# Kernel tuning notes

Hardware: AMD Instinct MI355X
Metric: run time of the kernel (lower is better)

Reference implementation:

```python
import jax, jax.numpy as jnp
import numpy as np
import math

B, T, P, E, H = 4, 64, 256, 512, 8
D = E // H
LN_EPS = 1e-5


def setup_inputs() -> dict:
    key = jax.random.key(0)
    ks = jax.random.split(key, 6)
    s = 0.02  # weight init scale
    return {
        "x": jax.random.normal(ks[0], (B, T, P, E), jnp.float32),
        "Wq": jax.random.normal(ks[1], (E, E), jnp.float32) * s,
        "bq": jnp.zeros((E,), jnp.float32),
        "Wk": jax.random.normal(ks[2], (E, E), jnp.float32) * s,
        "bk": jnp.zeros((E,), jnp.float32),
        "Wv": jax.random.normal(ks[3], (E, E), jnp.float32) * s,
        "bv": jnp.zeros((E,), jnp.float32),
        "Wo": jax.random.normal(ks[4], (E, E), jnp.float32) * s,
        "bo": jnp.zeros((E,), jnp.float32),
        "ln_g": jnp.ones((E,), jnp.float32),
        "ln_b": jnp.zeros((E,), jnp.float32),
    }


def _proj(x, W, b):
    # torch nn.Linear: y = x @ W.T + b
    return jnp.einsum('btpe,fe->btpf', x, W) + b


def _heads(y):
    # b t p (h d) -> b p h t d
    b, t, p, e = y.shape
    return y.reshape(b, t, p, H, D).transpose(0, 2, 3, 1, 4)


def reference(x, Wq, bq, Wk, bk, Wv, bv, Wo, bo, ln_g, ln_b):
    b, t, p, e = x.shape
    q = _heads(_proj(x, Wq, bq))  # [B,P,H,T,D]
    k = _heads(_proj(x, Wk, bk))
    v = _heads(_proj(x, Wv, bv))

    scores = jnp.einsum('bphtd,bphsd->bphts', q, k) / math.sqrt(D)
    causal_mask = jnp.triu(jnp.ones((t, t), dtype=bool), k=1)  # True above diag
    scores = jnp.where(causal_mask, -jnp.inf, scores)
    attn = jax.nn.softmax(scores, axis=-1)
    o = jnp.einsum('bphts,bphsd->bphtd', attn, v)

    # b p h t d -> b t p (h d)
    o = o.transpose(0, 3, 1, 2, 4).reshape(b, t, p, e)
    attn_out = jnp.einsum('btpe,fe->btpf', o, Wo) + bo

    y = x + attn_out
    # AdaptiveNormalizer with conditioning=None -> plain LayerNorm over E
    mu = jnp.mean(y, axis=-1, keepdims=True)
    var = jnp.var(y, axis=-1, keepdims=True)
    return (y - mu) * jax.lax.rsqrt(var + LN_EPS) * ln_g + ln_b
```

## Files before the change

### kernel.cpp

```cpp
#include <hip/hip_runtime.h>
#include <stdint.h>

#define B_ 4
#define T_ 64
#define P_ 256
#define E_ 512
#define H_ 8
#define D_ 64
#define NF 1536
#define MCH 16384

typedef unsigned short u16;
typedef __attribute__((ext_vector_type(8))) __bf16 bf16x8;
typedef __attribute__((ext_vector_type(4))) float f32x4;

__device__ __forceinline__ u16 f2bf(float x) {
  union { float f; uint32_t u; } a; a.f = x;
  uint32_t u = a.u;
  uint32_t r = (u + 0x7FFFu + ((u >> 16) & 1u)) >> 16;
  return (u16)r;
}

__device__ __forceinline__ bf16x8 ld8(const u16* p) {
  union { uint4 u; bf16x8 b; } t;
  t.u = *reinterpret_cast<const uint4*>(p);
  return t.b;
}

typedef __attribute__((address_space(3))) void lds_void;
typedef __attribute__((address_space(1))) void g_void;
__device__ __forceinline__ void gl_lds16(const void* g, void* l) {
  __builtin_amdgcn_global_load_lds((g_void*)g, (lds_void*)l, 16, 0, 0);
}

__device__ __forceinline__ f32x4 mfma16(bf16x8 a, bf16x8 b, f32x4 c) {
  return __builtin_amdgcn_mfma_f32_16x16x32_bf16(a, b, c, 0, 0, 0);
}

__global__ void cvt_bf16(const float* __restrict__ src, u16* __restrict__ dst, int n8) {
  int i = blockIdx.x * blockDim.x + threadIdx.x;
  if (i >= n8) return;
  const float4* s = reinterpret_cast<const float4*>(src) + (size_t)i * 2;
  float4 a = s[0], b = s[1];
  union { u16 u[8]; uint4 v; } t;
  t.u[0] = f2bf(a.x); t.u[1] = f2bf(a.y); t.u[2] = f2bf(a.z); t.u[3] = f2bf(a.w);
  t.u[4] = f2bf(b.x); t.u[5] = f2bf(b.y); t.u[6] = f2bf(b.z); t.u[7] = f2bf(b.w);
  reinterpret_cast<uint4*>(dst)[i] = t.v;
}

__global__ __launch_bounds__(256) void k1_qkv(
    const u16* __restrict__ xbf,
    const u16* __restrict__ wqkv,
    const float* __restrict__ bq, const float* __restrict__ bk, const float* __restrict__ bv,
    u16* __restrict__ qkv)
{
  __shared__ u16 As[128 * 64];
  __shared__ u16 Bs[128 * 64];
  const int tid = threadIdx.x;
  const int lane = tid & 63;
  const int wid = tid >> 6;
  const int m0 = blockIdx.y * 128;
  const int n0 = blockIdx.x * 128;
  const int wm = (wid >> 1) * 64;
  const int wn = (wid & 1) * 64;
  const int g4 = lane >> 4;

  f32x4 acc[4][4];
#pragma unroll
  for (int i = 0; i < 4; i++)
#pragma unroll
    for (int j = 0; j < 4; j++) { f32x4 z = {0.f, 0.f, 0.f, 0.f}; acc[i][j] = z; }

  const u16* ga = xbf + (size_t)m0 * E_;
  const u16* gb = wqkv + (size_t)n0 * E_;
  const int lrow = lane >> 3;
  const int lcol = (lane & 7) * 8;

  for (int kt = 0; kt < E_ / 64; ++kt) {
    const int k0 = kt * 64;
    __syncthreads();
#pragma unroll
    for (int p = 0; p < 4; ++p) {
      const int ch = wid * 4 + p;
      const int r = ch * 8 + lrow;
      gl_lds16(ga + (size_t)r * E_ + k0 + lcol, As + ch * 512);
      gl_lds16(gb + (size_t)r * E_ + k0 + lcol, Bs + ch * 512);
    }
    __syncthreads();
#pragma unroll
    for (int ks = 0; ks < 2; ++ks) {
      const int fc = ks * 32 + g4 * 8;
      bf16x8 af[4], bfr[4];
#pragma unroll
      for (int mi = 0; mi < 4; mi++) af[mi] = ld8(As + (wm + mi * 16 + (lane & 15)) * 64 + fc);
#pragma unroll
      for (int ni = 0; ni < 4; ni++) bfr[ni] = ld8(Bs + (wn + ni * 16 + (lane & 15)) * 64 + fc);
#pragma unroll
      for (int mi = 0; mi < 4; mi++)
#pragma unroll
        for (int ni = 0; ni < 4; ni++)
          acc[mi][ni] = mfma16(af[mi], bfr[ni], acc[mi][ni]);
    }
  }
#pragma unroll
  for (int ni = 0; ni < 4; ni++) {
    const int fcol = n0 + wn + ni * 16 + (lane & 15);
    const float bias = fcol < 512 ? bq[fcol] : (fcol < 1024 ? bk[fcol - 512] : bv[fcol - 1024]);
#pragma unroll
    for (int mi = 0; mi < 4; mi++)
#pragma unroll
      for (int r = 0; r < 4; r++) {
        const int row = m0 + wm + mi * 16 + g4 * 4 + r;
        qkv[(size_t)row * NF + fcol] = f2bf(acc[mi][ni][r] + bias);
      }
  }
}

__global__ __launch_bounds__(256) void k2_attn(
    const u16* __restrict__ qkv,
    u16* __restrict__ o)
{
  __shared__ u16 Pl[4][64 * 72];
  const int tid = threadIdx.x, lane = tid & 63, wid = tid >> 6;
  const int gw = blockIdx.x * 4 + wid;
  const int h = gw & 7, p = gw >> 3;
  const int g4 = lane >> 4;
  const size_t ts = (size_t)P_ * NF;
  const u16* qb = qkv + (size_t)p * NF + h * D_;
  const u16* kb = qb + 512;
  const u16* vb = qb + 1024;

  bf16x8 qf[4][2], kf[4][2];
#pragma unroll
  for (int i = 0; i < 4; i++)
#pragma unroll
    for (int ks = 0; ks < 2; ks++) {
      const int rr = i * 16 + (lane & 15);
      const int dc = ks * 32 + g4 * 8;
      qf[i][ks] = ld8(qb + (size_t)rr * ts + dc);
      kf[i][ks] = ld8(kb + (size_t)rr * ts + dc);
    }
  f32x4 S[4][4];
#pragma unroll
  for (int i = 0; i < 4; i++)
#pragma unroll
    for (int j = 0; j < 4; j++) { f32x4 z = {0.f, 0.f, 0.f, 0.f}; S[i][j] = z; }
#pragma unroll
  for (int ks = 0; ks < 2; ks++)
#pragma unroll
    for (int mi = 0; mi < 4; mi++)
#pragma unroll
      for (int ni = 0; ni < 4; ni++)
        S[mi][ni] = mfma16(qf[mi][ks], kf[ni][ks], S[mi][ni]);

  u16* pw = &Pl[wid][0];
#pragma unroll
  for (int mi = 0; mi < 4; mi++)
#pragma unroll
    for (int r = 0; r < 4; r++) {
      const int t = mi * 16 + g4 * 4 + r;
      float v[4]; float mx = -1e30f;
#pragma unroll
      for (int ni = 0; ni < 4; ni++) {
        const int s = ni * 16 + (lane & 15);
        v[ni] = (s <= t) ? S[mi][ni][r] * 0.125f : -1e30f;
        mx = fmaxf(mx, v[ni]);
      }
      mx = fmaxf(mx, __shfl_xor(mx, 1));
      mx = fmaxf(mx, __shfl_xor(mx, 2));
      mx = fmaxf(mx, __shfl_xor(mx, 4));
      mx = fmaxf(mx, __shfl_xor(mx, 8));
      float sum = 0.f; float pv[4];
#pragma unroll
      for (int ni = 0; ni < 4; ni++) {
        const int s = ni * 16 + (lane & 15);
        pv[ni] = (s <= t) ? __expf(v[ni] - mx) : 0.f;
        sum += pv[ni];
      }
      sum += __shfl_xor(sum, 1);
      sum += __shfl_xor(sum, 2);
      sum += __shfl_xor(sum, 4);
      sum += __shfl_xor(sum, 8);
      const float inv = 1.0f / sum;
#pragma unroll
      for (int ni = 0; ni < 4; ni++) {
        const int s = ni * 16 + (lane & 15);
        pw[t * 72 + s] = f2bf(pv[ni] * inv);
      }
    }
  __syncthreads();

  f32x4 O[4][4];
#pragma unroll
  for (int i = 0; i < 4; i++)
#pragma unroll
    for (int j = 0; j < 4; j++) { f32x4 z = {0.f, 0.f, 0.f, 0.f}; O[i][j] = z; }
#pragma unroll
  for (int ks = 0; ks < 2; ks++) {
    bf16x8 pa[4], vf[4];
#pragma unroll
    for (int mi = 0; mi < 4; mi++)
      pa[mi] = ld8(pw + (mi * 16 + (lane & 15)) * 72 + ks * 32 + g4 * 8);
#pragma unroll
    for (int ni = 0; ni < 4; ni++) {
      union { u16 u[8]; bf16x8 b; } tv;
#pragma unroll
      for (int j = 0; j < 8; j++) {
        const int s = ks * 32 + g4 * 8 + j;
        tv.u[j] = vb[(size_t)s * ts + ni * 16 + (lane & 15)];
      }
      vf[ni] = tv.b;
    }
#pragma unroll
    for (int mi = 0; mi < 4; mi++)
#pragma unroll
      for (int ni = 0; ni < 4; ni++)
        O[mi][ni] = mfma16(pa[mi], vf[ni], O[mi][ni]);
  }
#pragma unroll
  for (int mi = 0; mi < 4; mi++)
#pragma unroll
    for (int ni = 0; ni < 4; ni++)
#pragma unroll
      for (int r = 0; r < 4; r++) {
        const int t = mi * 16 + g4 * 4 + r;
        const int d = ni * 16 + (lane & 15);
        o[((size_t)t * P_ + p) * E_ + h * D_ + d] = f2bf(O[mi][ni][r]);
      }
}

__global__ __launch_bounds__(256) void k3_out(
    const u16* __restrict__ obf,
    const u16* __restrict__ wo,
    const float* __restrict__ bo,
    const float* __restrict__ x,
    const float* __restrict__ lng, const float* __restrict__ lnb,
    float* __restrict__ out)
{
  __shared__ u16 As[32 * 32];
  __shared__ u16 Bs[512 * 32];
  __shared__ float redS[32][4];
  __shared__ float redQ[32][4];
  const int tid = threadIdx.x, lane = tid & 63, wid = tid >> 6;
  const int m0 = blockIdx.x * 32;
  const int g4 = lane >> 4;
  const int lr = lane >> 2;
  const int lc = (lane & 3) * 8;

  f32x4 acc[2][8];
#pragma unroll
  for (int i = 0; i < 2; i++)
#pragma unroll
    for (int j = 0; j < 8; j++) { f32x4 z = {0.f, 0.f, 0.f, 0.f}; acc[i][j] = z; }

  const u16* ga = obf + (size_t)m0 * E_;

  for (int kt = 0; kt < 16; ++kt) {
    const int k0 = kt * 32;
    __syncthreads();
    if (wid < 2) {
      gl_lds16(ga + (size_t)(wid * 16 + lr) * E_ + k0 + lc, As + wid * 512);
    }
#pragma unroll
    for (int pass = 0; pass < 8; ++pass) {
      const int ch = wid * 8 + pass;
      gl_lds16(wo + (size_t)(ch * 16 + lr) * E_ + k0 + lc, Bs + ch * 512);
    }
    __syncthreads();
    const int fc = g4 * 8;
    bf16x8 af[2], bfr[8];
#pragma unroll
    for (int mi = 0; mi < 2; mi++) af[mi] = ld8(As + (mi * 16 + (lane & 15)) * 32 + fc);
#pragma unroll
    for (int ni = 0; ni < 8; ni++) bfr[ni] = ld8(Bs + (wid * 128 + ni * 16 + (lane & 15)) * 32 + fc);
#pragma unroll
    for (int mi = 0; mi < 2; mi++)
#pragma unroll
      for (int ni = 0; ni < 8; ni++)
        acc[mi][ni] = mfma16(af[mi], bfr[ni], acc[mi][ni]);
  }

  float gg[8], bb[8], bof[8];
#pragma unroll
  for (int ni = 0; ni < 8; ni++) {
    const int f = wid * 128 + ni * 16 + (lane & 15);
    gg[ni] = lng[f]; bb[ni] = lnb[f]; bof[ni] = bo[f];
  }
#pragma unroll
  for (int mi = 0; mi < 2; mi++)
#pragma unroll
    for (int r = 0; r < 4; r++) {
      const int n = m0 + mi * 16 + g4 * 4 + r;
#pragma unroll
      for (int ni = 0; ni < 8; ni++) {
        const int f = wid * 128 + ni * 16 + (lane & 15);
        acc[mi][ni][r] += bof[ni] + x[(size_t)n * E_ + f];
      }
    }
#pragma unroll
  for (int mi = 0; mi < 2; mi++)
#pragma unroll
    for (int r = 0; r < 4; r++) {
      float s = 0.f, q = 0.f;
#pragma unroll
      for (int ni = 0; ni < 8; ni++) { const float y = acc[mi][ni][r]; s += y; q += y * y; }
      s += __shfl_xor(s, 1); q += __shfl_xor(q, 1);
      s += __shfl_xor(s, 2); q += __shfl_xor(q, 2);
      s += __shfl_xor(s, 4); q += __shfl_xor(q, 4);
      s += __shfl_xor(s, 8); q += __shfl_xor(q, 8);
      if ((lane & 15) == 0) {
        const int rl = mi * 16 + g4 * 4 + r;
        redS[rl][wid] = s; redQ[rl][wid] = q;
      }
    }
  __syncthreads();
#pragma unroll
  for (int mi = 0; mi < 2; mi++)
#pragma unroll
    for (int r = 0; r < 4; r++) {
      const int rl = mi * 16 + g4 * 4 + r;
      const float Sx = redS[rl][0] + redS[rl][1] + redS[rl][2] + redS[rl][3];
      const float Qx = redQ[rl][0] + redQ[rl][1] + redQ[rl][2] + redQ[rl][3];
      const float mean = Sx * (1.0f / 512.0f);
      const float var = Qx * (1.0f / 512.0f) - mean * mean;
      const float rs = rsqrtf(var + 1e-5f);
      const int n = m0 + rl;
#pragma unroll
      for (int ni = 0; ni < 8; ni++) {
        const int f = wid * 128 + ni * 16 + (lane & 15);
        out[(size_t)n * E_ + f] = (acc[mi][ni][r] - mean) * rs * gg[ni] + bb[ni];
      }
    }
}

extern "C" void kernel_launch(void* const* d_in, const int* in_sizes, int n_in,
                              void* d_out, int out_size, void* d_ws, size_t ws_size,
                              hipStream_t stream) {
  const float* x   = (const float*)d_in[0];
  const float* Wq  = (const float*)d_in[1];
  const float* bq  = (const float*)d_in[2];
  const float* Wk  = (const float*)d_in[3];
  const float* bk  = (const float*)d_in[4];
  const float* Wv  = (const float*)d_in[5];
  const float* bv  = (const float*)d_in[6];
  const float* Wo  = (const float*)d_in[7];
  const float* bo  = (const float*)d_in[8];
  const float* lng = (const float*)d_in[9];
  const float* lnb = (const float*)d_in[10];
  float* out = (float*)d_out;

  uint8_t* ws = (uint8_t*)d_ws;
  u16* xbf  = (u16*)(ws);
  u16* qkvc = (u16*)(ws + 16777216);
  u16* obf  = (u16*)(ws + 67108864);
  u16* wqkv = (u16*)(ws + 83886080);
  u16* wobf = (u16*)(ws + 85458944);

  cvt_bf16<<<128, 256, 0, stream>>>(Wq, wqkv,               E_ * E_ / 8);
  cvt_bf16<<<128, 256, 0, stream>>>(Wk, wqkv + E_ * E_,     E_ * E_ / 8);
  cvt_bf16<<<128, 256, 0, stream>>>(Wv, wqkv + 2 * E_ * E_, E_ * E_ / 8);
  cvt_bf16<<<128, 256, 0, stream>>>(Wo, wobf,               E_ * E_ / 8);

  for (int b = 0; b < B_; ++b) {
    const float* xb = x + (size_t)b * MCH * E_;
    cvt_bf16<<<4096, 256, 0, stream>>>(xb, xbf, MCH * E_ / 8);
    k1_qkv<<<dim3(12, 128), 256, 0, stream>>>(xbf, wqkv, bq, bk, bv, qkvc);
    k2_attn<<<512, 256, 0, stream>>>(qkvc, obf);
    k3_out<<<512, 256, 0, stream>>>(obf, wobf, bo, xb, lng, lnb, out + (size_t)b * MCH * E_);
  }
}
```

Baseline: 426.9 us.

## Double-buffer GEMM tiles, enlarge out-proj tile, batch all launches when workspace allows

Measured after the change: 433.4 us. No clear change (+1.5%).

```diff
diff --git a/kernel.cpp b/kernel.cpp
--- a/kernel.cpp
+++ b/kernel.cpp
@@ -48,14 +48,30 @@
   reinterpret_cast<uint4*>(dst)[i] = t.v;
 }
 
+__global__ void cvt_w(const float* __restrict__ Wq, const float* __restrict__ Wk,
+                      const float* __restrict__ Wv, const float* __restrict__ Wo,
+                      u16* __restrict__ wqkv, u16* __restrict__ wobf) {
+  int idx = blockIdx.x * blockDim.x + threadIdx.x;
+  int w = idx >> 15;
+  int off = idx & 32767;
+  const float* s = (w == 0) ? Wq : (w == 1) ? Wk : (w == 2) ? Wv : Wo;
+  const float4* sp = reinterpret_cast<const float4*>(s) + (size_t)off * 2;
+  float4 a = sp[0], b = sp[1];
+  union { u16 u[8]; uint4 v; } t;
+  t.u[0] = f2bf(a.x); t.u[1] = f2bf(a.y); t.u[2] = f2bf(a.z); t.u[3] = f2bf(a.w);
+  t.u[4] = f2bf(b.x); t.u[5] = f2bf(b.y); t.u[6] = f2bf(b.z); t.u[7] = f2bf(b.w);
+  if (w < 3) reinterpret_cast<uint4*>(wqkv)[w * 32768 + off] = t.v;
+  else       reinterpret_cast<uint4*>(wobf)[off] = t.v;
+}
+
 __global__ __launch_bounds__(256) void k1_qkv(
     const u16* __restrict__ xbf,
     const u16* __restrict__ wqkv,
     const float* __restrict__ bq, const float* __restrict__ bk, const float* __restrict__ bv,
     u16* __restrict__ qkv)
 {
-  __shared__ u16 As[128 * 64];
-  __shared__ u16 Bs[128 * 64];
+  __shared__ u16 As[2][128 * 64];
+  __shared__ u16 Bs[2][128 * 64];
   const int tid = threadIdx.x;
   const int lane = tid & 63;
   const int wid = tid >> 6;
@@ -63,7 +79,9 @@
   const int n0 = blockIdx.x * 128;
   const int wm = (wid >> 1) * 64;
   const int wn = (wid & 1) * 64;
-  const int g4 = lane >> 4;
+  const int g4 = lane >> 4, l15 = lane & 15;
+  const int lrow = lane >> 3;
+  const int lcol = (lane & 7) * 8;
 
   f32x4 acc[4][4];
 #pragma unroll
@@ -73,38 +91,43 @@
 
   const u16* ga = xbf + (size_t)m0 * E_;
   const u16* gb = wqkv + (size_t)n0 * E_;
-  const int lrow = lane >> 3;
-  const int lcol = (lane & 7) * 8;
-
-  for (int kt = 0; kt < E_ / 64; ++kt) {
+
+  auto stage = [&](int buf, int kt) {
     const int k0 = kt * 64;
-    __syncthreads();
 #pragma unroll
     for (int p = 0; p < 4; ++p) {
       const int ch = wid * 4 + p;
       const int r = ch * 8 + lrow;
-      gl_lds16(ga + (size_t)r * E_ + k0 + lcol, As + ch * 512);
-      gl_lds16(gb + (size_t)r * E_ + k0 + lcol, Bs + ch * 512);
-    }
-    __syncthreads();
+      gl_lds16(ga + (size_t)r * E_ + k0 + lcol, &As[buf][ch * 512]);
+      gl_lds16(gb + (size_t)r * E_ + k0 + lcol, &Bs[buf][ch * 512]);
+    }
+  };
+
+  stage(0, 0);
+  __syncthreads();
+  int cur = 0;
+  for (int kt = 0; kt < 8; ++kt) {
+    if (kt < 7) stage(cur ^ 1, kt + 1);
 #pragma unroll
     for (int ks = 0; ks < 2; ++ks) {
       const int fc = ks * 32 + g4 * 8;
       bf16x8 af[4], bfr[4];
 #pragma unroll
-      for (int mi = 0; mi < 4; mi++) af[mi] = ld8(As + (wm + mi * 16 + (lane & 15)) * 64 + fc);
-#pragma unroll
-      for (int ni = 0; ni < 4; ni++) bfr[ni] = ld8(Bs + (wn + ni * 16 + (lane & 15)) * 64 + fc);
+      for (int mi = 0; mi < 4; mi++) af[mi] = ld8(&As[cur][(wm + mi * 16 + l15) * 64 + fc]);
+#pragma unroll
+      for (int ni = 0; ni < 4; ni++) bfr[ni] = ld8(&Bs[cur][(wn + ni * 16 + l15) * 64 + fc]);
 #pragma unroll
       for (int mi = 0; mi < 4; mi++)
 #pragma unroll
         for (int ni = 0; ni < 4; ni++)
           acc[mi][ni] = mfma16(af[mi], bfr[ni], acc[mi][ni]);
     }
+    __syncthreads();
+    cur ^= 1;
   }
 #pragma unroll
   for (int ni = 0; ni < 4; ni++) {
-    const int fcol = n0 + wn + ni * 16 + (lane & 15);
+    const int fcol = n0 + wn + ni * 16 + l15;
     const float bias = fcol < 512 ? bq[fcol] : (fcol < 1024 ? bk[fcol - 512] : bv[fcol - 1024]);
 #pragma unroll
     for (int mi = 0; mi < 4; mi++)
@@ -123,12 +146,15 @@
   __shared__ u16 Pl[4][64 * 72];
   const int tid = threadIdx.x, lane = tid & 63, wid = tid >> 6;
   const int gw = blockIdx.x * 4 + wid;
-  const int h = gw & 7, p = gw >> 3;
+  const int b = gw >> 11;
+  const int g = gw & 2047;
+  const int h = g & 7, p = g >> 3;
   const int g4 = lane >> 4;
   const size_t ts = (size_t)P_ * NF;
-  const u16* qb = qkv + (size_t)p * NF + h * D_;
+  const u16* qb = qkv + (size_t)b * MCH * NF + (size_t)p * NF + h * D_;
   const u16* kb = qb + 512;
   const u16* vb = qb + 1024;
+  u16* ob = o + (size_t)b * MCH * E_;
 
   bf16x8 qf[4][2], kf[4][2];
 #pragma unroll
@@ -225,11 +251,11 @@
       for (int r = 0; r < 4; r++) {
         const int t = mi * 16 + g4 * 4 + r;
         const int d = ni * 16 + (lane & 15);
-        o[((size_t)t * P_ + p) * E_ + h * D_ + d] = f2bf(O[mi][ni][r]);
-      }
-}
-
-__global__ __launch_bounds__(256) void k3_out(
+        ob[((size_t)t * P_ + p) * E_ + h * D_ + d] = f2bf(O[mi][ni][r]);
+      }
+}
+
+__global__ __launch_bounds__(512) void k3_out(
     const u16* __restrict__ obf,
     const u16* __restrict__ wo,
     const float* __restrict__ bo,
@@ -237,97 +263,103 @@
     const float* __restrict__ lng, const float* __restrict__ lnb,
     float* __restrict__ out)
 {
-  __shared__ u16 As[32 * 32];
-  __shared__ u16 Bs[512 * 32];
-  __shared__ float redS[32][4];
-  __shared__ float redQ[32][4];
+  __shared__ u16 As[2][128 * 32];
+  __shared__ u16 Bs[2][512 * 32];
+  __shared__ float redS[128][8];
+  __shared__ float redQ[128][8];
   const int tid = threadIdx.x, lane = tid & 63, wid = tid >> 6;
-  const int m0 = blockIdx.x * 32;
-  const int g4 = lane >> 4;
+  const int m0 = blockIdx.x * 128;
+  const int g4 = lane >> 4, l15 = lane & 15;
   const int lr = lane >> 2;
   const int lc = (lane & 3) * 8;
 
-  f32x4 acc[2][8];
-#pragma unroll
-  for (int i = 0; i < 2; i++)
-#pragma unroll
-    for (int j = 0; j < 8; j++) { f32x4 z = {0.f, 0.f, 0.f, 0.f}; acc[i][j] = z; }
+  f32x4 acc[8][4];
+#pragma unroll
+  for (int i = 0; i < 8; i++)
+#pragma unroll
+    for (int j = 0; j < 4; j++) { f32x4 z = {0.f, 0.f, 0.f, 0.f}; acc[i][j] = z; }
 
   const u16* ga = obf + (size_t)m0 * E_;
 
+  auto stage = [&](int buf, int kt) {
+    const int k0 = kt * 32;
+    gl_lds16(ga + (size_t)(wid * 16 + lr) * E_ + k0 + lc, &As[buf][wid * 512]);
+#pragma unroll
+    for (int p = 0; p < 4; ++p) {
+      const int ch = wid * 4 + p;
+      gl_lds16(wo + (size_t)(ch * 16 + lr) * E_ + k0 + lc, &Bs[buf][ch * 512]);
+    }
+  };
+
+  stage(0, 0);
+  __syncthreads();
+  int cur = 0;
   for (int kt = 0; kt < 16; ++kt) {
-    const int k0 = kt * 32;
+    if (kt < 15) stage(cur ^ 1, kt + 1);
+    const int fc = g4 * 8;
+    bf16x8 af[8], bfr[4];
+#pragma unroll
+    for (int mi = 0; mi < 8; mi++) af[mi] = ld8(&As[cur][(mi * 16 + l15) * 32 + fc]);
+#pragma unroll
+    for (int ni = 0; ni < 4; ni++) bfr[ni] = ld8(&Bs[cur][(wid * 64 + ni * 16 + l15) * 32 + fc]);
+#pragma unroll
+    for (int mi = 0; mi < 8; mi++)
+#pragma unroll
+      for (int ni = 0; ni < 4; ni++)
+        acc[mi][ni] = mfma16(af[mi], bfr[ni], acc[mi][ni]);
     __syncthreads();
-    if (wid < 2) {
-      gl_lds16(ga + (size_t)(wid * 16 + lr) * E_ + k0 + lc, As + wid * 512);
-    }
-#pragma unroll
-    for (int pass = 0; pass < 8; ++pass) {
-      const int ch = wid * 8 + pass;
-      gl_lds16(wo + (size_t)(ch * 16 + lr) * E_ + k0 + lc, Bs + ch * 512);
-    }
-    __syncthreads();
-    const int fc = g4 * 8;
-    bf16x8 af[2], bfr[8];
-#pragma unroll
-    for (int mi = 0; mi < 2; mi++) af[mi] = ld8(As + (mi * 16 + (lane & 15)) * 32 + fc);
-#pragma unroll
-    for (int ni = 0; ni < 8; ni++) bfr[ni] = ld8(Bs + (wid * 128 + ni * 16 + (lane & 15)) * 32 + fc);
-#pragma unroll
-    for (int mi = 0; mi < 2; mi++)
-#pragma unroll
-      for (int ni = 0; ni < 8; ni++)
-        acc[mi][ni] = mfma16(af[mi], bfr[ni], acc[mi][ni]);
-  }
-
-  float gg[8], bb[8], bof[8];
-#pragma unroll
-  for (int ni = 0; ni < 8; ni++) {
-    const int f = wid * 128 + ni * 16 + (lane & 15);
+    cur ^= 1;
+  }
+
+  float gg[4], bb[4], bof[4];
+#pragma unroll
+  for (int ni = 0; ni < 4; ni++) {
+    const int f = wid * 64 + ni * 16 + l15;
     gg[ni] = lng[f]; bb[ni] = lnb[f]; bof[ni] = bo[f];
   }
 #pragma unroll
-  for (int mi = 0; mi < 2; mi++)
+  for (int mi = 0; mi < 8; mi++)
 #pragma unroll
     for (int r = 0; r < 4; r++) {
       const int n = m0 + mi * 16 + g4 * 4 + r;
 #pragma unroll
-      for (int ni = 0; ni < 8; ni++) {
-        const int f = wid * 128 + ni * 16 + (lane & 15);
+      for (int ni = 0; ni < 4; ni++) {
+        const int f = wid * 64 + ni * 16 + l15;
         acc[mi][ni][r] += bof[ni] + x[(size_t)n * E_ + f];
       }
     }
 #pragma unroll
-  for (int mi = 0; mi < 2; mi++)
+  for (int mi = 0; mi < 8; mi++)
 #pragma unroll
     for (int r = 0; r < 4; r++) {
       float s = 0.f, q = 0.f;
 #pragma unroll
-      for (int ni = 0; ni < 8; ni++) { const float y = acc[mi][ni][r]; s += y; q += y * y; }
+      for (int ni = 0; ni < 4; ni++) { const float y = acc[mi][ni][r]; s += y; q += y * y; }
       s += __shfl_xor(s, 1); q += __shfl_xor(q, 1);
       s += __shfl_xor(s, 2); q += __shfl_xor(q, 2);
       s += __shfl_xor(s, 4); q += __shfl_xor(q, 4);
       s += __shfl_xor(s, 8); q += __shfl_xor(q, 8);
-      if ((lane & 15) == 0) {
+      if (l15 == 0) {
         const int rl = mi * 16 + g4 * 4 + r;
         redS[rl][wid] = s; redQ[rl][wid] = q;
       }
     }
   __syncthreads();
 #pragma unroll
-  for (int mi = 0; mi < 2; mi++)
+  for (int mi = 0; mi < 8; mi++)
 #pragma unroll
     for (int r = 0; r < 4; r++) {
       const int rl = mi * 16 + g4 * 4 + r;
-      const float Sx = redS[rl][0] + redS[rl][1] + redS[rl][2] + redS[rl][3];
-      const float Qx = redQ[rl][0] + redQ[rl][1] + redQ[rl][2] + redQ[rl][3];
+      float Sx = 0.f, Qx = 0.f;
+#pragma unroll
+      for (int w = 0; w < 8; w++) { Sx += redS[rl][w]; Qx += redQ[rl][w]; }
       const float mean = Sx * (1.0f / 512.0f);
       const float var = Qx * (1.0f / 512.0f) - mean * mean;
       const float rs = rsqrtf(var + 1e-5f);
       const int n = m0 + rl;
 #pragma unroll
-      for (int ni = 0; ni < 8; ni++) {
-        const int f = wid * 128 + ni * 16 + (lane & 15);
+      for (int ni = 0; ni < 4; ni++) {
+        const int f = wid * 64 + ni * 16 + l15;
         out[(size_t)n * E_ + f] = (acc[mi][ni][r] - mean) * rs * gg[ni] + bb[ni];
       }
     }
@@ -348,24 +380,35 @@
   const float* lng = (const float*)d_in[9];
   const float* lnb = (const float*)d_in[10];
   float* out = (float*)d_out;
-
   uint8_t* ws = (uint8_t*)d_ws;
-  u16* xbf  = (u16*)(ws);
-  u16* qkvc = (u16*)(ws + 16777216);
-  u16* obf  = (u16*)(ws + 67108864);
-  u16* wqkv = (u16*)(ws + 83886080);
-  u16* wobf = (u16*)(ws + 85458944);
-
-  cvt_bf16<<<128, 256, 0, stream>>>(Wq, wqkv,               E_ * E_ / 8);
-  cvt_bf16<<<128, 256, 0, stream>>>(Wk, wqkv + E_ * E_,     E_ * E_ / 8);
-  cvt_bf16<<<128, 256, 0, stream>>>(Wv, wqkv + 2 * E_ * E_, E_ * E_ / 8);
-  cvt_bf16<<<128, 256, 0, stream>>>(Wo, wobf,               E_ * E_ / 8);
-
-  for (int b = 0; b < B_; ++b) {
-    const float* xb = x + (size_t)b * MCH * E_;
-    cvt_bf16<<<4096, 256, 0, stream>>>(xb, xbf, MCH * E_ / 8);
-    k1_qkv<<<dim3(12, 128), 256, 0, stream>>>(xbf, wqkv, bq, bk, bv, qkvc);
-    k2_attn<<<512, 256, 0, stream>>>(qkvc, obf);
-    k3_out<<<512, 256, 0, stream>>>(obf, wobf, bo, xb, lng, lnb, out + (size_t)b * MCH * E_);
-  }
-}
+
+  const size_t NEED_BIG = 270532608ULL;
+  if (ws_size >= NEED_BIG) {
+    u16* wqkv = (u16*)(ws);
+    u16* wobf = (u16*)(ws + 1572864);
+    u16* xbf  = (u16*)(ws + 2097152);
+    u16* qkvc = (u16*)(ws + 69206016);
+    u16* obf  = xbf;
+
+    cvt_w<<<512, 256, 0, stream>>>(Wq, Wk, Wv, Wo, wqkv, wobf);
+    cvt_bf16<<<16384, 256, 0, stream>>>(x, xbf, B_ * MCH * E_ / 8);
+    k1_qkv<<<dim3(12, 512), 256, 0, stream>>>(xbf, wqkv, bq, bk, bv, qkvc);
+    k2_attn<<<2048, 256, 0, stream>>>(qkvc, obf);
+    k3_out<<<512, 512, 0, stream>>>(obf, wobf, bo, x, lng, lnb, out);
+  } else {
+    u16* xbf  = (u16*)(ws);
+    u16* qkvc = (u16*)(ws + 16777216);
+    u16* obf  = (u16*)(ws + 67108864);
+    u16* wqkv = (u16*)(ws + 83886080);
+    u16* wobf = (u16*)(ws + 85458944);
+
+    cvt_w<<<512, 256, 0, stream>>>(Wq, Wk, Wv, Wo, wqkv, wobf);
+    for (int b = 0; b < B_; ++b) {
+      const float* xb = x + (size_t)b * MCH * E_;
+      cvt_bf16<<<4096, 256, 0, stream>>>(xb, xbf, MCH * E_ / 8);
+      k1_qkv<<<dim3(12, 128), 256, 0, stream>>>(xbf, wqkv, bq, bk, bv, qkvc);
+      k2_attn<<<512, 256, 0, stream>>>(qkvc, obf);
+      k3_out<<<128, 512, 0, stream>>>(obf, wobf, bo, xb, lng, lnb, out + (size_t)b * MCH * E_);
+    }
+  }
+}
```
